# Kernel tuning notes

Measured on AMD Instinct MI355X. Metric: run time of the kernel, lower is better.

## Reference

```python
import jax, jax.numpy as jnp
import numpy as np

T, B, L, D, A = 64, 64, 100, 128, 18
H = 4 * D  # lstm_size = 4 * input_size


def lstm_cell(x, h, c, Wih, Whh, bih, bhh):
    # PyTorch LSTM gate order: i, f, g, o
    g = x @ Wih.T + bih + h @ Whh.T + bhh
    i, f, gg, o = jnp.split(g, 4, axis=-1)
    c = jax.nn.sigmoid(f) * c + jax.nn.sigmoid(i) * jnp.tanh(gg)
    h = jax.nn.sigmoid(o) * jnp.tanh(c)
    return h, c


def setup_inputs() -> dict:
    key = jax.random.key(0)
    ks = jax.random.split(key, 26)

    def gl(k, shape, fan_in):
        s = float(1.0 / np.sqrt(fan_in))
        return jax.random.uniform(k, shape, jnp.float32, -s, s)

    return dict(
        state=jax.random.normal(ks[0], (T, B, D), jnp.float32),
        demonstration=jax.random.normal(ks[1], (T, B, L, D), jnp.float32),
        demonstration_length=jax.random.randint(ks[2], (T, B), 1, L + 1),
        prev_action=jax.random.randint(ks[3], (T, B), 0, A),
        prev_reward=jax.random.normal(ks[4], (T, B), jnp.float32),
        h0=jnp.zeros((B, H), jnp.float32),
        c0=jnp.zeros((B, H), jnp.float32),
        enc_Wih=gl(ks[5], (4 * H, D), H), enc_Whh=gl(ks[6], (4 * H, H), H),
        enc_bih=gl(ks[7], (4 * H,), H), enc_bhh=gl(ks[8], (4 * H,), H),
        attn_W=gl(ks[9], (H, H), H), attn_b=gl(ks[10], (H,), H),
        comb_W=gl(ks[11], (H, D + H), D + H), comb_b=gl(ks[12], (H,), D + H),
        lstm_Wih=gl(ks[13], (4 * H, H), H), lstm_Whh=gl(ks[14], (4 * H, H), H),
        lstm_bih=gl(ks[15], (4 * H,), H), lstm_bhh=gl(ks[16], (4 * H,), H),
        mid_W=gl(ks[17], (H, H), H), mid_b=gl(ks[18], (H,), H),
        out_W=gl(ks[19], (A, H), H), out_b=gl(ks[20], (A,), H),
    )


def reference(state, demonstration, demonstration_length, prev_action, prev_reward,
              h0, c0, enc_Wih, enc_Whh, enc_bih, enc_bhh, attn_W, attn_b,
              comb_W, comb_b, lstm_Wih, lstm_Whh, lstm_bih, lstm_bhh,
              mid_W, mid_b, out_W, out_b):
    Lm = demonstration.shape[2]
    demo0 = demonstration[0]  # [B, L, D] (source uses demonstration[0] only)

    # --- demonstration encoder LSTM over L, zero initial state ---
    def enc_step(carry, x):
        h, c = carry
        h, c = lstm_cell(x, h, c, enc_Wih, enc_Whh, enc_bih, enc_bhh)
        return (h, c), h

    z = jnp.zeros((demo0.shape[0], H), demo0.dtype)
    _, enc = jax.lax.scan(enc_step, (z, z), jnp.swapaxes(demo0, 0, 1))
    enc = jnp.swapaxes(enc, 0, 1)  # [B, L, H]

    # invariant across t in the source loop; hoisted (same math)
    attn_proj = enc @ attn_W.T + attn_b  # [B, L, H]
    lengths = demonstration_length[0]  # [B]
    mask = jnp.arange(Lm)[None, :] < lengths[:, None]  # [B, L]
    scale = jnp.float32(1.0 / np.sqrt(Lm))

    # --- per-timestep fused attention + LSTM cell + heads ---
    def step(carry, obs_t):
        h, c = carry
        w = jnp.einsum('blh,bh->bl', attn_proj, h) * scale
        w = jnp.where(mask, w, -jnp.inf)
        w = jax.nn.softmax(w, axis=-1)
        applied = jnp.einsum('bl,blh->bh', w, enc)
        x = jax.nn.relu(jnp.concatenate([applied, obs_t], axis=-1) @ comb_W.T + comb_b)
        h, c = lstm_cell(x, h, c, lstm_Wih, lstm_Whh, lstm_bih, lstm_bhh)
        m = h @ mid_W.T + mid_b
        q_t = m @ out_W.T + out_b
        return (h, c), q_t

    (h, c), q = jax.lax.scan(step, (h0, c0), state)  # q: [T, B, A]
    return q, h, c
```

## Files before the change

kernel.cpp:

```cpp
#include <hip/hip_runtime.h>
#include <math.h>

#define Bsz 64
#define Tn 64
#define Ln 100
#define Dn 128
#define An 18
#define Hn 512
#define NGRP 16

__device__ __forceinline__ float sigf(float x){ return 1.0f/(1.0f+expf(-x)); }

__device__ __forceinline__ void scst(float* p, float v){
  __hip_atomic_store(p, v, __ATOMIC_RELAXED, __HIP_MEMORY_SCOPE_AGENT);
}
__device__ __forceinline__ void scsti(int* p, int v){
  __hip_atomic_store(p, v, __ATOMIC_RELAXED, __HIP_MEMORY_SCOPE_AGENT);
}
__device__ __forceinline__ int lcldi(const int* p){
  return __hip_atomic_load((int*)p, __ATOMIC_RELAXED, __HIP_MEMORY_SCOPE_AGENT);
}

__device__ __forceinline__ void gbar_arrive(int* grp_arr, int* grp_gen, int* root, int nb, int ph){
  const int gs = nb >> 4;
  const int g  = (int)blockIdx.x & 15;
  int a = __hip_atomic_fetch_add(grp_arr + g*64, 1, __ATOMIC_RELAXED, __HIP_MEMORY_SCOPE_AGENT) + 1;
  if (a == ph*gs){
    int r = __hip_atomic_fetch_add(root, 1, __ATOMIC_RELAXED, __HIP_MEMORY_SCOPE_AGENT) + 1;
    if (r == ph*NGRP){
      #pragma unroll
      for (int i = 0; i < NGRP; i++) scsti(grp_gen + i*64, ph);
    }
  }
}
__device__ __forceinline__ void gbar_wait(int* grp_gen, int ph){
  const int g = (int)blockIdx.x & 15;
  while (lcldi(grp_gen + g*64) < ph) __builtin_amdgcn_s_sleep(1);
}
__device__ __forceinline__ void gbarH(int* gA, int* gG, int* gR, int nb, int ph){
  __syncthreads();
  if (threadIdx.x == 0){
    asm volatile("s_waitcnt vmcnt(0) lgkmcnt(0)" ::: "memory");
    gbar_arrive(gA, gG, gR, nb, ph);
    gbar_wait(gG, ph);
  }
  __syncthreads();
}

__global__ __launch_bounds__(256) void demo_transpose_kernel(
    const float* __restrict__ demo, float* __restrict__ demoT)
{
  int idx = blockIdx.x*256 + threadIdx.x;
  if (idx < Ln*Bsz*Dn) {
    int d = idx & 127;
    int b = (idx >> 7) & 63;
    int l = idx >> 13;
    demoT[idx] = demo[((size_t)(b*Ln + l))*Dn + d];
  }
}

__global__ __launch_bounds__(256) void gemm_nt_kernel(
    const float* __restrict__ A, int lda,
    const float* __restrict__ B, int ldb,
    const float* __restrict__ bias,
    float* __restrict__ C, int ldc, int K)
{
  __shared__ float As[64][17];
  __shared__ float Bs[64][17];
  const int m0 = blockIdx.x * 64;
  const int n0 = blockIdx.y * 64;
  const int tx = threadIdx.x & 15;
  const int ty = threadIdx.x >> 4;
  float acc[4][4] = {};
  for (int k0 = 0; k0 < K; k0 += 16) {
    #pragma unroll
    for (int i = 0; i < 4; i++) {
      int e = threadIdx.x + i*256;
      int r = e >> 4, c = e & 15;
      As[r][c] = A[(size_t)(m0 + r)*lda + k0 + c];
      Bs[r][c] = B[(size_t)(n0 + r)*ldb + k0 + c];
    }
    __syncthreads();
    #pragma unroll
    for (int kk = 0; kk < 16; kk++) {
      float a0 = As[ty*4+0][kk], a1 = As[ty*4+1][kk], a2 = As[ty*4+2][kk], a3 = As[ty*4+3][kk];
      float b0 = Bs[tx*4+0][kk], b1 = Bs[tx*4+1][kk], b2 = Bs[tx*4+2][kk], b3 = Bs[tx*4+3][kk];
      acc[0][0] += a0*b0; acc[0][1] += a0*b1; acc[0][2] += a0*b2; acc[0][3] += a0*b3;
      acc[1][0] += a1*b0; acc[1][1] += a1*b1; acc[1][2] += a1*b2; acc[1][3] += a1*b3;
      acc[2][0] += a2*b0; acc[2][1] += a2*b1; acc[2][2] += a2*b2; acc[2][3] += a2*b3;
      acc[3][0] += a3*b0; acc[3][1] += a3*b1; acc[3][2] += a3*b2; acc[3][3] += a3*b3;
    }
    __syncthreads();
  }
  #pragma unroll
  for (int i = 0; i < 4; i++) {
    #pragma unroll
    for (int j = 0; j < 4; j++) {
      int nn = n0 + tx*4 + j;
      float v = acc[i][j] + (bias ? bias[nn] : 0.0f);
      C[(size_t)(m0 + ty*4 + i)*ldc + nn] = v;
    }
  }
}

__global__ __launch_bounds__(512) void head_fold_kernel(
    const float* __restrict__ mid_W, const float* __restrict__ mid_b,
    const float* __restrict__ out_W, const float* __restrict__ out_b,
    float* __restrict__ M2, float* __restrict__ bias2)
{
  const int a = blockIdx.x;
  const int k = threadIdx.x;
  const float* ow = out_W + (size_t)a*Hn;
  float s = 0.f;
  #pragma unroll 4
  for (int n = 0; n < Hn; n++) s += ow[n]*mid_W[(size_t)n*Hn + k];
  M2[(size_t)a*Hn + k] = s;
  if (k == 0){
    float b2 = out_b[a];
    for (int n = 0; n < Hn; n++) b2 += ow[n]*mid_b[n];
    bias2[a] = b2;
  }
}

__global__ __launch_bounds__(256) void qhead_kernel(
    const float* __restrict__ hhist, const float* __restrict__ M2,
    const float* __restrict__ bias2, float* __restrict__ q)
{
  const int t = blockIdx.x;
  for (int p = threadIdx.x; p < Bsz*An; p += 256){
    int b = p / An, a = p % An;
    const float4* hv = (const float4*)(hhist + ((size_t)t*Bsz + b)*Hn);
    const float4* mv = (const float4*)(M2 + (size_t)a*Hn);
    float s = bias2[a];
    #pragma unroll 8
    for (int k = 0; k < Hn/4; k++){
      float4 H = hv[k], M = mv[k];
      s += H.x*M.x + H.y*M.y + H.z*M.z + H.w*M.w;
    }
    q[((size_t)(t*Bsz + b))*An + a] = s;
  }
}

__global__ __launch_bounds__(512, 1) void enc_scan_kernel(
    const float* __restrict__ demoT,
    const float* __restrict__ Wih, const float* __restrict__ Whh,
    const float* __restrict__ bih, const float* __restrict__ bhh,
    const float* __restrict__ attn_W, const float* __restrict__ attn_b,
    const float* __restrict__ comb_W,
    float* __restrict__ hencR,
    float* __restrict__ attnp,
    float* __restrict__ CE,
    int* __restrict__ gA, int* __restrict__ gG, int* __restrict__ gR)
{
  const int bid  = blockIdx.x;
  const int tid  = threadIdx.x;
  const int lane = tid & 63;
  const int ks   = tid >> 6;
  const int n0   = bid*2;

  __shared__ float lds_whh[8][Hn];
  __shared__ float lds_wih[8][Dn];
  __shared__ float lds_atw[2][Hn];
  __shared__ float lds_cbw[2][Hn];
  __shared__ float red[8][12][Bsz];

  #pragma unroll
  for (int c = 0; c < 2; c++)
    #pragma unroll
    for (int g = 0; g < 4; g++){
      int r = c*4 + g;
      lds_whh[r][tid] = Whh[(size_t)(g*Hn + n0 + c)*Hn + tid];
      if (tid < Dn) lds_wih[r][tid] = Wih[(size_t)(g*Hn + n0 + c)*Dn + tid];
    }
  #pragma unroll
  for (int c = 0; c < 2; c++){
    lds_atw[c][tid] = attn_W[(size_t)(n0 + c)*Hn + tid];
    lds_cbw[c][tid] = comb_W[(size_t)(n0 + c)*(Hn + Dn) + tid];
  }
  float bsum[2][4];
  #pragma unroll
  for (int c = 0; c < 2; c++)
    #pragma unroll
    for (int g = 0; g < 4; g++){
      int r = g*Hn + n0 + c;
      bsum[c][g] = bih[r] + bhh[r];
    }
  const float ab[2] = { attn_b[n0], attn_b[n0+1] };
  float cr[2] = {0.f, 0.f};
  __syncthreads();

  for (int l = 0; l <= Ln; l++){
    if (l < Ln){
      float a[2][4] = {{0,0,0,0},{0,0,0,0}};
      if (l >= 1){
        const float4* hv = (const float4*)(hencR + ((size_t)(l-1)*Bsz + lane)*Hn) + ks*16;
        #pragma unroll 4
        for (int q = 0; q < 16; q++){
          float4 H = hv[q];
          #pragma unroll
          for (int c = 0; c < 2; c++)
            #pragma unroll
            for (int g = 0; g < 4; g++){
              float4 W = *(const float4*)&lds_whh[c*4+g][ks*64 + 4*q];
              a[c][g] += H.x*W.x + H.y*W.y + H.z*W.z + H.w*W.w;
            }
        }
      }
      {
        const float4* dv = (const float4*)(demoT + ((size_t)l*Bsz + lane)*Dn) + ks*4;
        #pragma unroll
        for (int q = 0; q < 4; q++){
          float4 V = dv[q];
          #pragma unroll
          for (int c = 0; c < 2; c++)
            #pragma unroll
            for (int g = 0; g < 4; g++){
              float4 W = *(const float4*)&lds_wih[c*4+g][ks*16 + 4*q];
              a[c][g] += V.x*W.x + V.y*W.y + V.z*W.z + V.w*W.w;
            }
        }
      }
      #pragma unroll
      for (int c = 0; c < 2; c++)
        #pragma unroll
        for (int g = 0; g < 4; g++) red[ks][c*4+g][lane] = a[c][g];
      __syncthreads();
      if (tid < Bsz){
        int b = tid;
        #pragma unroll
        for (int c = 0; c < 2; c++){
          float g0 = bsum[c][0], g1 = bsum[c][1], g2 = bsum[c][2], g3 = bsum[c][3];
          #pragma unroll
          for (int k = 0; k < 8; k++){
            g0 += red[k][c*4+0][b]; g1 += red[k][c*4+1][b];
            g2 += red[k][c*4+2][b]; g3 += red[k][c*4+3][b];
          }
          float ii = sigf(g0), ff = sigf(g1), gg = tanhf(g2), oo = sigf(g3);
          float cn = ff*cr[c] + ii*gg;
          float hn = oo*tanhf(cn);
          cr[c] = cn;
          scst(hencR + ((size_t)l*Bsz + b)*Hn + n0 + c, hn);
        }
      }
      if (tid == 0){
        asm volatile("s_waitcnt vmcnt(0)" ::: "memory");
        gbar_arrive(gA, gG, gR, (int)gridDim.x, l+1);
      }
    }
    if (l >= 1){
      float aa[2] = {0,0}, ac[2] = {0,0};
      const float4* hv = (const float4*)(hencR + ((size_t)(l-1)*Bsz + lane)*Hn) + ks*16;
      #pragma unroll 4
      for (int q = 0; q < 16; q++){
        float4 H = hv[q];
        #pragma unroll
        for (int c = 0; c < 2; c++){
          float4 Aw = *(const float4*)&lds_atw[c][ks*64 + 4*q];
          aa[c] += H.x*Aw.x + H.y*Aw.y + H.z*Aw.z + H.w*Aw.w;
          float4 Cw = *(const float4*)&lds_cbw[c][ks*64 + 4*q];
          ac[c] += H.x*Cw.x + H.y*Cw.y + H.z*Cw.z + H.w*Cw.w;
        }
      }
      #pragma unroll
      for (int c = 0; c < 2; c++){
        red[ks][8+c][lane]  = aa[c];
        red[ks][10+c][lane] = ac[c];
      }
      __syncthreads();
      if (tid < Bsz){
        int b = tid;
        #pragma unroll
        for (int c = 0; c < 2; c++){
          float av = ab[c], cv = 0.f;
          #pragma unroll
          for (int k = 0; k < 8; k++){ av += red[k][8+c][b]; cv += red[k][10+c][b]; }
          scst(attnp + ((size_t)(b*Ln + (l-1)))*Hn + n0 + c, av);
          scst(CE    + ((size_t)(b*Ln + (l-1)))*Hn + n0 + c, cv);
        }
      }
    }
    if (l < Ln){
      if (tid == 0) gbar_wait(gG, l+1);
      __syncthreads();
    }
  }
}

__global__ __launch_bounds__(512, 1) void dec_scan_kernel(
    const float* __restrict__ h0, const float* __restrict__ c0,
    const float* __restrict__ attnp,
    const float* __restrict__ CE,
    const float* __restrict__ preobs,
    const int*   __restrict__ dlen,
    const float* __restrict__ lstm_Wih, const float* __restrict__ lstm_Whh,
    const float* __restrict__ lstm_bih, const float* __restrict__ lstm_bhh,
    const float* __restrict__ comb_b,
    float* __restrict__ xrow,
    float* __restrict__ hhist,
    float* __restrict__ outp,
    int* __restrict__ gA, int* __restrict__ gG, int* __restrict__ gR)
{
  const int bid  = blockIdx.x;
  const int tid  = threadIdx.x;
  const int lane = tid & 63;
  const int ks   = tid >> 6;
  const int n0   = bid*2;

  __shared__ float lds_wi[8][Hn];
  __shared__ float lds_wh[8][Hn];
  __shared__ float hs[Hn];
  __shared__ float wls[128];
  __shared__ float mx_s, sum_s;
  __shared__ float red[8][8][Bsz];

  #pragma unroll
  for (int c = 0; c < 2; c++)
    #pragma unroll
    for (int g = 0; g < 4; g++){
      int r = c*4 + g;
      lds_wi[r][tid] = lstm_Wih[(size_t)(g*Hn + n0 + c)*Hn + tid];
      lds_wh[r][tid] = lstm_Whh[(size_t)(g*Hn + n0 + c)*Hn + tid];
    }
  float bs[2][4];
  #pragma unroll
  for (int c = 0; c < 2; c++)
    #pragma unroll
    for (int g = 0; g < 4; g++){
      int r = g*Hn + n0 + c;
      bs[c][g] = lstm_bih[r] + lstm_bhh[r];
    }
  float cr[2] = {0.f, 0.f};
  int ph = 0;
  __syncthreads();

  for (int t = 0; t < Tn; t++){
    const float* hprev_all = (t == 0) ? h0 : (hhist + (size_t)(t-1)*Bsz*Hn);

    if (bid < Bsz){
      const int b = bid;
      hs[tid] = hprev_all[(size_t)b*Hn + tid];
      if (tid >= 100 && tid < 128) wls[tid] = -1e30f;
      __syncthreads();
      const int len = dlen[b];
      if (tid < 400){
        int l = tid >> 2, kh = tid & 3;
        const float4* ap = (const float4*)(attnp + ((size_t)(b*Ln + l))*Hn) + kh*32;
        const float4* hv = (const float4*)hs + kh*32;
        float s = 0.f;
        #pragma unroll 8
        for (int k = 0; k < 32; k++){
          float4 A = ap[k], H = hv[k];
          s += A.x*H.x + A.y*H.y + A.z*H.z + A.w*H.w;
        }
        s += __shfl_xor(s, 1);
        s += __shfl_xor(s, 2);
        if (kh == 0) wls[l] = (l < len) ? s*0.1f : -1e30f;
      }
      __syncthreads();
      if (tid < 64){
        float v = fmaxf(wls[tid], wls[tid+64]);
        for (int off = 1; off < 64; off <<= 1) v = fmaxf(v, __shfl_xor(v, off));
        if (tid == 0) mx_s = v;
      }
      __syncthreads();
      float mx = mx_s;
      if (tid < 64){
        float e0 = (wls[tid]    > -1e29f) ? expf(wls[tid]    - mx) : 0.f;
        float e1 = (wls[tid+64] > -1e29f) ? expf(wls[tid+64] - mx) : 0.f;
        wls[tid] = e0; wls[tid+64] = e1;
        float v = e0 + e1;
        for (int off = 1; off < 64; off <<= 1) v += __shfl_xor(v, off);
        if (tid == 0) sum_s = v;
      }
      __syncthreads();
      float inv = 1.0f / sum_s;
      {
        int n = tid;
        const float* cb = CE + (size_t)b*Ln*Hn + n;
        float acc = 0.f;
        #pragma unroll 4
        for (int l2 = 0; l2 < Ln; ++l2) acc += cb[(size_t)l2*Hn]*wls[l2];
        float v = acc*inv + preobs[((size_t)(t*Bsz + b))*Hn + n] + comb_b[n];
        scst(xrow + ((size_t)t*Bsz + b)*Hn + n, fmaxf(v, 0.f));
      }
    }
    float hpa[2][4] = {{0,0,0,0},{0,0,0,0}};
    {
      const float4* hv = (const float4*)(hprev_all + (size_t)lane*Hn) + ks*16;
      #pragma unroll 4
      for (int q = 0; q < 16; q++){
        float4 H = hv[q];
        #pragma unroll
        for (int c = 0; c < 2; c++)
          #pragma unroll
          for (int g = 0; g < 4; g++){
            float4 W = *(const float4*)&lds_wh[c*4+g][ks*64 + 4*q];
            hpa[c][g] += H.x*W.x + H.y*W.y + H.z*W.z + H.w*W.w;
          }
      }
    }
    gbarH(gA, gG, gR, (int)gridDim.x, ++ph);

    {
      const float4* xv = (const float4*)(xrow + ((size_t)t*Bsz + lane)*Hn) + ks*16;
      #pragma unroll 4
      for (int q = 0; q < 16; q++){
        float4 X = xv[q];
        #pragma unroll
        for (int c = 0; c < 2; c++)
          #pragma unroll
          for (int g = 0; g < 4; g++){
            float4 W = *(const float4*)&lds_wi[c*4+g][ks*64 + 4*q];
            hpa[c][g] += X.x*W.x + X.y*W.y + X.z*W.z + X.w*W.w;
          }
      }
      #pragma unroll
      for (int c = 0; c < 2; c++)
        #pragma unroll
        for (int g = 0; g < 4; g++) red[ks][c*4+g][lane] = hpa[c][g];
      __syncthreads();
      if (tid < Bsz){
        int b = tid;
        #pragma unroll
        for (int c = 0; c < 2; c++){
          int n = n0 + c;
          if (t == 0) cr[c] = c0[(size_t)b*Hn + n];
          float g0 = bs[c][0], g1 = bs[c][1], g2 = bs[c][2], g3 = bs[c][3];
          #pragma unroll
          for (int k = 0; k < 8; k++){
            g0 += red[k][c*4+0][b]; g1 += red[k][c*4+1][b];
            g2 += red[k][c*4+2][b]; g3 += red[k][c*4+3][b];
          }
          float ii = sigf(g0), ff = sigf(g1), gg = tanhf(g2), oo = sigf(g3);
          float cn = ff*cr[c] + ii*gg;
          float hn = oo*tanhf(cn);
          cr[c] = cn;
          scst(hhist + ((size_t)t*Bsz + b)*Hn + n, hn);
          if (t == Tn - 1){
            outp[Tn*Bsz*An + (size_t)b*Hn + n]           = hn;
            outp[Tn*Bsz*An + Bsz*Hn + (size_t)b*Hn + n]  = cn;
          }
        }
      }
      if (t < Tn - 1){
        if (tid == 0){
          asm volatile("s_waitcnt vmcnt(0)" ::: "memory");
          gbar_arrive(gA, gG, gR, (int)gridDim.x, ph+1);
          gbar_wait(gG, ph+1);
        }
        ph++;
        __syncthreads();
      }
    }
  }
}

extern "C" void kernel_launch(void* const* d_in, const int* in_sizes, int n_in,
                              void* d_out, int out_size, void* d_ws, size_t ws_size,
                              hipStream_t stream) {
  (void)in_sizes; (void)n_in; (void)out_size; (void)ws_size;
  const float* state    = (const float*)d_in[0];
  const float* demo     = (const float*)d_in[1];
  const int*   dlen     = (const int*)  d_in[2];
  const float* h0       = (const float*)d_in[5];
  const float* c0       = (const float*)d_in[6];
  const float* enc_Wih  = (const float*)d_in[7];
  const float* enc_Whh  = (const float*)d_in[8];
  const float* enc_bih  = (const float*)d_in[9];
  const float* enc_bhh  = (const float*)d_in[10];
  const float* attn_W   = (const float*)d_in[11];
  const float* attn_b   = (const float*)d_in[12];
  const float* comb_W   = (const float*)d_in[13];
  const float* comb_b   = (const float*)d_in[14];
  const float* lstm_Wih = (const float*)d_in[15];
  const float* lstm_Whh = (const float*)d_in[16];
  const float* lstm_bih = (const float*)d_in[17];
  const float* lstm_bhh = (const float*)d_in[18];
  const float* mid_W    = (const float*)d_in[19];
  const float* mid_b    = (const float*)d_in[20];
  const float* out_W    = (const float*)d_in[21];
  const float* out_b    = (const float*)d_in[22];
  float* ws   = (float*)d_ws;
  float* qout = (float*)d_out;

  float* attnp  = ws + 0;
  float* CE     = ws + 3276800;
  float* preobs = ws + 6553600;
  float* region = ws + 8650752;
  float* demoT  = region;
  float* hencR  = region + 819200;
  float* xrow   = region;
  float* hhist  = region + 2097152;
  int*   barB   = (int*)(ws + 12845056);
  int* encA = barB;          int* encG = barB + 1024; int* encR = barB + 2048;
  int* decA = barB + 2112;   int* decG = barB + 3136; int* decR = barB + 4160;
  float* M2    = ws + 12850176;
  float* bias2 = ws + 12859392;

  hipMemsetAsync((void*)barB, 0, 4224*4, stream);

  demo_transpose_kernel<<<3200, 256, 0, stream>>>(demo, demoT);

  head_fold_kernel<<<An, 512, 0, stream>>>(mid_W, mid_b, out_W, out_b, M2, bias2);

  gemm_nt_kernel<<<dim3(Tn*Bsz/64, Hn/64), 256, 0, stream>>>(
      state, Dn, comb_W + Hn, Hn + Dn, nullptr, preobs, Hn, Dn);

  enc_scan_kernel<<<256, 512, 0, stream>>>(
      demoT, enc_Wih, enc_Whh, enc_bih, enc_bhh, attn_W, attn_b, comb_W,
      hencR, attnp, CE, encA, encG, encR);

  dec_scan_kernel<<<256, 512, 0, stream>>>(
      h0, c0, attnp, CE, preobs, dlen, lstm_Wih, lstm_Whh, lstm_bih, lstm_bhh,
      comb_b, xrow, hhist, qout, decA, decG, decR);

  qhead_kernel<<<Tn, 256, 0, stream>>>(hhist, M2, bias2, qout);
}
```

Measured before the change: 3.418 ms.

## Split decoder attention across 128 blocks with partial softmax merge; fuse encoder projections

In the decoder, the attention and context computation for each batch row is split over two blocks, each handling 50 positions. Each block writes a partial max, denominator and weighted context, and these are merged flash-style when the LSTM input is built after the grid barrier. This halves the serial attention work per block that sits before the barrier, at the cost of extra global traffic and redundant merging in every block. In the encoder, the attention and combine projections of the previous step are folded into the same h-vector pass as the recurrent matmul. That removes one h reload and one __syncthreads per step.

```diff
diff --git a/kernel.cpp b/kernel.cpp
--- a/kernel.cpp
+++ b/kernel.cpp
@@ -190,93 +190,79 @@
   __syncthreads();
 
   for (int l = 0; l <= Ln; l++){
-    if (l < Ln){
-      float a[2][4] = {{0,0,0,0},{0,0,0,0}};
-      if (l >= 1){
-        const float4* hv = (const float4*)(hencR + ((size_t)(l-1)*Bsz + lane)*Hn) + ks*16;
-        #pragma unroll 4
-        for (int q = 0; q < 16; q++){
-          float4 H = hv[q];
-          #pragma unroll
-          for (int c = 0; c < 2; c++)
-            #pragma unroll
-            for (int g = 0; g < 4; g++){
-              float4 W = *(const float4*)&lds_whh[c*4+g][ks*64 + 4*q];
-              a[c][g] += H.x*W.x + H.y*W.y + H.z*W.z + H.w*W.w;
-            }
-        }
-      }
-      {
-        const float4* dv = (const float4*)(demoT + ((size_t)l*Bsz + lane)*Dn) + ks*4;
-        #pragma unroll
-        for (int q = 0; q < 4; q++){
-          float4 V = dv[q];
-          #pragma unroll
-          for (int c = 0; c < 2; c++)
-            #pragma unroll
-            for (int g = 0; g < 4; g++){
-              float4 W = *(const float4*)&lds_wih[c*4+g][ks*16 + 4*q];
-              a[c][g] += V.x*W.x + V.y*W.y + V.z*W.z + V.w*W.w;
-            }
-        }
-      }
-      #pragma unroll
-      for (int c = 0; c < 2; c++)
-        #pragma unroll
-        for (int g = 0; g < 4; g++) red[ks][c*4+g][lane] = a[c][g];
-      __syncthreads();
-      if (tid < Bsz){
-        int b = tid;
-        #pragma unroll
-        for (int c = 0; c < 2; c++){
-          float g0 = bsum[c][0], g1 = bsum[c][1], g2 = bsum[c][2], g3 = bsum[c][3];
-          #pragma unroll
-          for (int k = 0; k < 8; k++){
-            g0 += red[k][c*4+0][b]; g1 += red[k][c*4+1][b];
-            g2 += red[k][c*4+2][b]; g3 += red[k][c*4+3][b];
-          }
-          float ii = sigf(g0), ff = sigf(g1), gg = tanhf(g2), oo = sigf(g3);
-          float cn = ff*cr[c] + ii*gg;
-          float hn = oo*tanhf(cn);
-          cr[c] = cn;
-          scst(hencR + ((size_t)l*Bsz + b)*Hn + n0 + c, hn);
-        }
-      }
-      if (tid == 0){
-        asm volatile("s_waitcnt vmcnt(0)" ::: "memory");
-        gbar_arrive(gA, gG, gR, (int)gridDim.x, l+1);
-      }
-    }
+    float a[2][4] = {{0,0,0,0},{0,0,0,0}};
+    float aa[2] = {0,0}, ac[2] = {0,0};
     if (l >= 1){
-      float aa[2] = {0,0}, ac[2] = {0,0};
       const float4* hv = (const float4*)(hencR + ((size_t)(l-1)*Bsz + lane)*Hn) + ks*16;
       #pragma unroll 4
       for (int q = 0; q < 16; q++){
         float4 H = hv[q];
         #pragma unroll
         for (int c = 0; c < 2; c++){
+          #pragma unroll
+          for (int g = 0; g < 4; g++){
+            float4 W = *(const float4*)&lds_whh[c*4+g][ks*64 + 4*q];
+            a[c][g] += H.x*W.x + H.y*W.y + H.z*W.z + H.w*W.w;
+          }
           float4 Aw = *(const float4*)&lds_atw[c][ks*64 + 4*q];
           aa[c] += H.x*Aw.x + H.y*Aw.y + H.z*Aw.z + H.w*Aw.w;
           float4 Cw = *(const float4*)&lds_cbw[c][ks*64 + 4*q];
           ac[c] += H.x*Cw.x + H.y*Cw.y + H.z*Cw.z + H.w*Cw.w;
         }
       }
+    }
+    if (l < Ln){
+      const float4* dv = (const float4*)(demoT + ((size_t)l*Bsz + lane)*Dn) + ks*4;
+      #pragma unroll
+      for (int q = 0; q < 4; q++){
+        float4 V = dv[q];
+        #pragma unroll
+        for (int c = 0; c < 2; c++)
+          #pragma unroll
+          for (int g = 0; g < 4; g++){
+            float4 W = *(const float4*)&lds_wih[c*4+g][ks*16 + 4*q];
+            a[c][g] += V.x*W.x + V.y*W.y + V.z*W.z + V.w*W.w;
+          }
+      }
+    }
+    #pragma unroll
+    for (int c = 0; c < 2; c++){
+      #pragma unroll
+      for (int g = 0; g < 4; g++) red[ks][c*4+g][lane] = a[c][g];
+      red[ks][8+c][lane]  = aa[c];
+      red[ks][10+c][lane] = ac[c];
+    }
+    __syncthreads();
+    if (tid < Bsz && l < Ln){
+      int b = tid;
       #pragma unroll
       for (int c = 0; c < 2; c++){
-        red[ks][8+c][lane]  = aa[c];
-        red[ks][10+c][lane] = ac[c];
-      }
-      __syncthreads();
-      if (tid < Bsz){
-        int b = tid;
-        #pragma unroll
-        for (int c = 0; c < 2; c++){
-          float av = ab[c], cv = 0.f;
-          #pragma unroll
-          for (int k = 0; k < 8; k++){ av += red[k][8+c][b]; cv += red[k][10+c][b]; }
-          scst(attnp + ((size_t)(b*Ln + (l-1)))*Hn + n0 + c, av);
-          scst(CE    + ((size_t)(b*Ln + (l-1)))*Hn + n0 + c, cv);
+        float g0 = bsum[c][0], g1 = bsum[c][1], g2 = bsum[c][2], g3 = bsum[c][3];
+        #pragma unroll
+        for (int k = 0; k < 8; k++){
+          g0 += red[k][c*4+0][b]; g1 += red[k][c*4+1][b];
+          g2 += red[k][c*4+2][b]; g3 += red[k][c*4+3][b];
         }
+        float ii = sigf(g0), ff = sigf(g1), gg = tanhf(g2), oo = sigf(g3);
+        float cn = ff*cr[c] + ii*gg;
+        float hn = oo*tanhf(cn);
+        cr[c] = cn;
+        scst(hencR + ((size_t)l*Bsz + b)*Hn + n0 + c, hn);
+      }
+    }
+    if (l < Ln && tid == 0){
+      asm volatile("s_waitcnt vmcnt(0)" ::: "memory");
+      gbar_arrive(gA, gG, gR, (int)gridDim.x, l+1);
+    }
+    if (tid < Bsz && l >= 1){
+      int b = tid;
+      #pragma unroll
+      for (int c = 0; c < 2; c++){
+        float av = ab[c], cv = 0.f;
+        #pragma unroll
+        for (int k = 0; k < 8; k++){ av += red[k][8+c][b]; cv += red[k][10+c][b]; }
+        scst(attnp + ((size_t)(b*Ln + (l-1)))*Hn + n0 + c, av);
+        scst(CE    + ((size_t)(b*Ln + (l-1)))*Hn + n0 + c, cv);
       }
     }
     if (l < Ln){
@@ -295,7 +281,9 @@
     const float* __restrict__ lstm_Wih, const float* __restrict__ lstm_Whh,
     const float* __restrict__ lstm_bih, const float* __restrict__ lstm_bhh,
     const float* __restrict__ comb_b,
-    float* __restrict__ xrow,
+    float* __restrict__ app,
+    float* __restrict__ dmax,
+    float* __restrict__ dden,
     float* __restrict__ hhist,
     float* __restrict__ outp,
     int* __restrict__ gA, int* __restrict__ gG, int* __restrict__ gR)
@@ -309,8 +297,9 @@
   __shared__ float lds_wi[8][Hn];
   __shared__ float lds_wh[8][Hn];
   __shared__ float hs[Hn];
-  __shared__ float wls[128];
-  __shared__ float mx_s, sum_s;
+  __shared__ float cbs[Hn];
+  __shared__ float sls[64];
+  __shared__ float wls[64];
   __shared__ float red[8][8][Bsz];
 
   #pragma unroll
@@ -321,6 +310,7 @@
       lds_wi[r][tid] = lstm_Wih[(size_t)(g*Hn + n0 + c)*Hn + tid];
       lds_wh[r][tid] = lstm_Whh[(size_t)(g*Hn + n0 + c)*Hn + tid];
     }
+  cbs[tid] = comb_b[tid];
   float bs[2][4];
   #pragma unroll
   for (int c = 0; c < 2; c++)
@@ -333,57 +323,14 @@
   int ph = 0;
   __syncthreads();
 
+  const int batn = bid & 63;
+  const int qq   = bid >> 6;
+
   for (int t = 0; t < Tn; t++){
     const float* hprev_all = (t == 0) ? h0 : (hhist + (size_t)(t-1)*Bsz*Hn);
 
-    if (bid < Bsz){
-      const int b = bid;
-      hs[tid] = hprev_all[(size_t)b*Hn + tid];
-      if (tid >= 100 && tid < 128) wls[tid] = -1e30f;
-      __syncthreads();
-      const int len = dlen[b];
-      if (tid < 400){
-        int l = tid >> 2, kh = tid & 3;
-        const float4* ap = (const float4*)(attnp + ((size_t)(b*Ln + l))*Hn) + kh*32;
-        const float4* hv = (const float4*)hs + kh*32;
-        float s = 0.f;
-        #pragma unroll 8
-        for (int k = 0; k < 32; k++){
-          float4 A = ap[k], H = hv[k];
-          s += A.x*H.x + A.y*H.y + A.z*H.z + A.w*H.w;
-        }
-        s += __shfl_xor(s, 1);
-        s += __shfl_xor(s, 2);
-        if (kh == 0) wls[l] = (l < len) ? s*0.1f : -1e30f;
-      }
-      __syncthreads();
-      if (tid < 64){
-        float v = fmaxf(wls[tid], wls[tid+64]);
-        for (int off = 1; off < 64; off <<= 1) v = fmaxf(v, __shfl_xor(v, off));
-        if (tid == 0) mx_s = v;
-      }
-      __syncthreads();
-      float mx = mx_s;
-      if (tid < 64){
-        float e0 = (wls[tid]    > -1e29f) ? expf(wls[tid]    - mx) : 0.f;
-        float e1 = (wls[tid+64] > -1e29f) ? expf(wls[tid+64] - mx) : 0.f;
-        wls[tid] = e0; wls[tid+64] = e1;
-        float v = e0 + e1;
-        for (int off = 1; off < 64; off <<= 1) v += __shfl_xor(v, off);
-        if (tid == 0) sum_s = v;
-      }
-      __syncthreads();
-      float inv = 1.0f / sum_s;
-      {
-        int n = tid;
-        const float* cb = CE + (size_t)b*Ln*Hn + n;
-        float acc = 0.f;
-        #pragma unroll 4
-        for (int l2 = 0; l2 < Ln; ++l2) acc += cb[(size_t)l2*Hn]*wls[l2];
-        float v = acc*inv + preobs[((size_t)(t*Bsz + b))*Hn + n] + comb_b[n];
-        scst(xrow + ((size_t)t*Bsz + b)*Hn + n, fmaxf(v, 0.f));
-      }
-    }
+    if (bid < 128) hs[tid] = hprev_all[(size_t)batn*Hn + tid];
+
     float hpa[2][4] = {{0,0,0,0},{0,0,0,0}};
     {
       const float4* hv = (const float4*)(hprev_all + (size_t)lane*Hn) + ks*16;
@@ -399,13 +346,77 @@
           }
       }
     }
+
+    if (bid < 128){
+      const int b = batn;
+      const int l0 = qq*50;
+      __syncthreads();
+      const int len = dlen[b];
+      const int li = tid >> 3, sub = tid & 7;
+      float s = -1e30f;
+      if (li < 50){
+        const float4* ap = (const float4*)(attnp + ((size_t)(b*Ln + l0 + li))*Hn) + sub*16;
+        const float4* hv2 = (const float4*)hs + sub*16;
+        float acc = 0.f;
+        #pragma unroll
+        for (int k = 0; k < 16; k++){
+          float4 A = ap[k], H = hv2[k];
+          acc += A.x*H.x + A.y*H.y + A.z*H.z + A.w*H.w;
+        }
+        acc += __shfl_xor(acc, 1);
+        acc += __shfl_xor(acc, 2);
+        acc += __shfl_xor(acc, 4);
+        s = acc;
+      }
+      if (sub == 0) sls[li] = (li < 50 && (l0 + li) < len) ? s*0.1f : -1e30f;
+      __syncthreads();
+      if (tid < 64){
+        float v = sls[tid];
+        float m = v;
+        #pragma unroll
+        for (int off = 1; off < 64; off <<= 1) m = fmaxf(m, __shfl_xor(m, off));
+        float w = expf(v - m);
+        wls[tid] = w;
+        float dsum = w;
+        #pragma unroll
+        for (int off = 1; off < 64; off <<= 1) dsum += __shfl_xor(dsum, off);
+        if (tid == 0){
+          scst(dmax + ((size_t)t*2 + qq)*Bsz + b, m);
+          scst(dden + ((size_t)t*2 + qq)*Bsz + b, dsum);
+        }
+      }
+      __syncthreads();
+      {
+        const int n = tid;
+        const float* ceb = CE + ((size_t)(b*Ln + l0))*Hn + n;
+        float apv = 0.f;
+        #pragma unroll 5
+        for (int l2 = 0; l2 < 50; l2++) apv += wls[l2]*ceb[(size_t)l2*Hn];
+        scst(app + (((size_t)t*2 + qq)*Bsz + b)*Hn + n, apv);
+      }
+    }
     gbarH(gA, gG, gR, (int)gridDim.x, ++ph);
 
     {
-      const float4* xv = (const float4*)(xrow + ((size_t)t*Bsz + lane)*Hn) + ks*16;
+      const size_t i0 = ((size_t)t*2 + 0)*Bsz + lane;
+      const size_t i1 = ((size_t)t*2 + 1)*Bsz + lane;
+      float m0 = dmax[i0], m1 = dmax[i1], d0v = dden[i0], d1v = dden[i1];
+      float M  = fmaxf(m0, m1);
+      float e0 = expf(m0 - M), e1 = expf(m1 - M);
+      float D  = e0*d0v + e1*d1v;
+      float s0 = e0/D, s1 = e1/D;
+      const float4* a0v = (const float4*)(app + i0*Hn) + ks*16;
+      const float4* a1v = (const float4*)(app + i1*Hn) + ks*16;
+      const float4* pv  = (const float4*)(preobs + ((size_t)t*Bsz + lane)*Hn) + ks*16;
       #pragma unroll 4
       for (int q = 0; q < 16; q++){
-        float4 X = xv[q];
+        float4 A0 = a0v[q], A1 = a1v[q], P = pv[q];
+        float4 CB = *(const float4*)&cbs[ks*64 + 4*q];
+        float4 X;
+        X.x = fmaxf(s0*A0.x + s1*A1.x + P.x + CB.x, 0.f);
+        X.y = fmaxf(s0*A0.y + s1*A1.y + P.y + CB.y, 0.f);
+        X.z = fmaxf(s0*A0.z + s1*A1.z + P.z + CB.z, 0.f);
+        X.w = fmaxf(s0*A0.w + s1*A1.w + P.w + CB.w, 0.f);
         #pragma unroll
         for (int c = 0; c < 2; c++)
           #pragma unroll
@@ -489,13 +500,15 @@
   float* region = ws + 8650752;
   float* demoT  = region;
   float* hencR  = region + 819200;
-  float* xrow   = region;
-  float* hhist  = region + 2097152;
-  int*   barB   = (int*)(ws + 12845056);
+  float* hhist  = region;
+  float* app    = region + 2097152;
+  float* dmax   = region + 6291456;
+  float* dden   = region + 6299648;
+  int*   barB   = (int*)(ws + 14958592);
   int* encA = barB;          int* encG = barB + 1024; int* encR = barB + 2048;
   int* decA = barB + 2112;   int* decG = barB + 3136; int* decR = barB + 4160;
-  float* M2    = ws + 12850176;
-  float* bias2 = ws + 12859392;
+  float* M2    = ws + 14962816;
+  float* bias2 = ws + 14972032;
 
   hipMemsetAsync((void*)barB, 0, 4224*4, stream);
 
@@ -512,7 +525,7 @@
 
   dec_scan_kernel<<<256, 512, 0, stream>>>(
       h0, c0, attnp, CE, preobs, dlen, lstm_Wih, lstm_Whh, lstm_bih, lstm_bhh,
-      comb_b, xrow, hhist, qout, decA, decG, decR);
+      comb_b, app, dmax, dden, hhist, qout, decA, decG, decR);
 
   qhead_kernel<<<Tn, 256, 0, stream>>>(hhist, M2, bias2, qout);
 }
```

After: 3.178 ms. -7.0%, faster.

## Merge encoder projection pass into recurrence step and trim attention loop to length

Applied to the files above, without the earlier changes.

In the encoder scan, the attention and combine projections of h_{l-1} are now computed in the same pass over h as the recurrent matvec. This removes one extra __syncthreads and one reload of h per step, and both results share one reduction. Both scans now use a gbarH helper for the grid barrier. The decoder's weighted sum over the encoder outputs stops at the demonstration length rounded up to a multiple of 8 instead of all 100 positions, with a deeper unroll. The workspace layout is changed so the buffers no longer alias, which adds memory footprint.

```diff
diff --git a/kernel.cpp b/kernel.cpp
--- a/kernel.cpp
+++ b/kernel.cpp
@@ -190,43 +190,52 @@
   __syncthreads();
 
   for (int l = 0; l <= Ln; l++){
+    float a[2][4] = {{0,0,0,0},{0,0,0,0}};
+    float aa[2] = {0,0}, ac[2] = {0,0};
+    if (l >= 1){
+      const float4* hv = (const float4*)(hencR + ((size_t)(l-1)*Bsz + lane)*Hn) + ks*16;
+      #pragma unroll 4
+      for (int q = 0; q < 16; q++){
+        float4 H = hv[q];
+        #pragma unroll
+        for (int c = 0; c < 2; c++){
+          #pragma unroll
+          for (int g = 0; g < 4; g++){
+            float4 W = *(const float4*)&lds_whh[c*4+g][ks*64 + 4*q];
+            a[c][g] += H.x*W.x + H.y*W.y + H.z*W.z + H.w*W.w;
+          }
+          float4 Aw = *(const float4*)&lds_atw[c][ks*64 + 4*q];
+          aa[c] += H.x*Aw.x + H.y*Aw.y + H.z*Aw.z + H.w*Aw.w;
+          float4 Cw = *(const float4*)&lds_cbw[c][ks*64 + 4*q];
+          ac[c] += H.x*Cw.x + H.y*Cw.y + H.z*Cw.z + H.w*Cw.w;
+        }
+      }
+    }
     if (l < Ln){
-      float a[2][4] = {{0,0,0,0},{0,0,0,0}};
-      if (l >= 1){
-        const float4* hv = (const float4*)(hencR + ((size_t)(l-1)*Bsz + lane)*Hn) + ks*16;
-        #pragma unroll 4
-        for (int q = 0; q < 16; q++){
-          float4 H = hv[q];
-          #pragma unroll
-          for (int c = 0; c < 2; c++)
-            #pragma unroll
-            for (int g = 0; g < 4; g++){
-              float4 W = *(const float4*)&lds_whh[c*4+g][ks*64 + 4*q];
-              a[c][g] += H.x*W.x + H.y*W.y + H.z*W.z + H.w*W.w;
-            }
-        }
-      }
-      {
-        const float4* dv = (const float4*)(demoT + ((size_t)l*Bsz + lane)*Dn) + ks*4;
-        #pragma unroll
-        for (int q = 0; q < 4; q++){
-          float4 V = dv[q];
-          #pragma unroll
-          for (int c = 0; c < 2; c++)
-            #pragma unroll
-            for (int g = 0; g < 4; g++){
-              float4 W = *(const float4*)&lds_wih[c*4+g][ks*16 + 4*q];
-              a[c][g] += V.x*W.x + V.y*W.y + V.z*W.z + V.w*W.w;
-            }
-        }
-      }
+      const float4* dv = (const float4*)(demoT + ((size_t)l*Bsz + lane)*Dn) + ks*4;
       #pragma unroll
-      for (int c = 0; c < 2; c++)
-        #pragma unroll
-        for (int g = 0; g < 4; g++) red[ks][c*4+g][lane] = a[c][g];
-      __syncthreads();
-      if (tid < Bsz){
-        int b = tid;
+      for (int q = 0; q < 4; q++){
+        float4 V = dv[q];
+        #pragma unroll
+        for (int c = 0; c < 2; c++)
+          #pragma unroll
+          for (int g = 0; g < 4; g++){
+            float4 W = *(const float4*)&lds_wih[c*4+g][ks*16 + 4*q];
+            a[c][g] += V.x*W.x + V.y*W.y + V.z*W.z + V.w*W.w;
+          }
+      }
+    }
+    #pragma unroll
+    for (int c = 0; c < 2; c++){
+      #pragma unroll
+      for (int g = 0; g < 4; g++) red[ks][c*4+g][lane] = a[c][g];
+      red[ks][8+c][lane]  = aa[c];
+      red[ks][10+c][lane] = ac[c];
+    }
+    __syncthreads();
+    if (tid < Bsz){
+      int b = tid;
+      if (l < Ln){
         #pragma unroll
         for (int c = 0; c < 2; c++){
           float g0 = bsum[c][0], g1 = bsum[c][1], g2 = bsum[c][2], g3 = bsum[c][3];
@@ -242,33 +251,7 @@
           scst(hencR + ((size_t)l*Bsz + b)*Hn + n0 + c, hn);
         }
       }
-      if (tid == 0){
-        asm volatile("s_waitcnt vmcnt(0)" ::: "memory");
-        gbar_arrive(gA, gG, gR, (int)gridDim.x, l+1);
-      }
-    }
-    if (l >= 1){
-      float aa[2] = {0,0}, ac[2] = {0,0};
-      const float4* hv = (const float4*)(hencR + ((size_t)(l-1)*Bsz + lane)*Hn) + ks*16;
-      #pragma unroll 4
-      for (int q = 0; q < 16; q++){
-        float4 H = hv[q];
-        #pragma unroll
-        for (int c = 0; c < 2; c++){
-          float4 Aw = *(const float4*)&lds_atw[c][ks*64 + 4*q];
-          aa[c] += H.x*Aw.x + H.y*Aw.y + H.z*Aw.z + H.w*Aw.w;
-          float4 Cw = *(const float4*)&lds_cbw[c][ks*64 + 4*q];
-          ac[c] += H.x*Cw.x + H.y*Cw.y + H.z*Cw.z + H.w*Cw.w;
-        }
-      }
-      #pragma unroll
-      for (int c = 0; c < 2; c++){
-        red[ks][8+c][lane]  = aa[c];
-        red[ks][10+c][lane] = ac[c];
-      }
-      __syncthreads();
-      if (tid < Bsz){
-        int b = tid;
+      if (l >= 1){
         #pragma unroll
         for (int c = 0; c < 2; c++){
           float av = ab[c], cv = 0.f;
@@ -279,10 +262,7 @@
         }
       }
     }
-    if (l < Ln){
-      if (tid == 0) gbar_wait(gG, l+1);
-      __syncthreads();
-    }
+    if (l < Ln) gbarH(gA, gG, gR, (int)gridDim.x, l+1);
   }
 }
 
@@ -330,6 +310,8 @@
       bs[c][g] = lstm_bih[r] + lstm_bhh[r];
     }
   float cr[2] = {0.f, 0.f};
+  int len = 0, lenr = 0;
+  if (bid < Bsz){ len = dlen[bid]; lenr = (len + 7) & ~7; }
   int ph = 0;
   __syncthreads();
 
@@ -341,7 +323,6 @@
       hs[tid] = hprev_all[(size_t)b*Hn + tid];
       if (tid >= 100 && tid < 128) wls[tid] = -1e30f;
       __syncthreads();
-      const int len = dlen[b];
       if (tid < 400){
         int l = tid >> 2, kh = tid & 3;
         const float4* ap = (const float4*)(attnp + ((size_t)(b*Ln + l))*Hn) + kh*32;
@@ -378,8 +359,8 @@
         int n = tid;
         const float* cb = CE + (size_t)b*Ln*Hn + n;
         float acc = 0.f;
-        #pragma unroll 4
-        for (int l2 = 0; l2 < Ln; ++l2) acc += cb[(size_t)l2*Hn]*wls[l2];
+        #pragma unroll 8
+        for (int l2 = 0; l2 < lenr; ++l2) acc += cb[(size_t)l2*Hn]*wls[l2];
         float v = acc*inv + preobs[((size_t)(t*Bsz + b))*Hn + n] + comb_b[n];
         scst(xrow + ((size_t)t*Bsz + b)*Hn + n, fmaxf(v, 0.f));
       }
@@ -442,16 +423,8 @@
           }
         }
       }
-      if (t < Tn - 1){
-        if (tid == 0){
-          asm volatile("s_waitcnt vmcnt(0)" ::: "memory");
-          gbar_arrive(gA, gG, gR, (int)gridDim.x, ph+1);
-          gbar_wait(gG, ph+1);
-        }
-        ph++;
-        __syncthreads();
-      }
-    }
+    }
+    if (t < Tn - 1) gbarH(gA, gG, gR, (int)gridDim.x, ++ph);
   }
 }
 
@@ -485,17 +458,16 @@
 
   float* attnp  = ws + 0;
   float* CE     = ws + 3276800;
-  float* preobs = ws + 6553600;
-  float* region = ws + 8650752;
-  float* demoT  = region;
-  float* hencR  = region + 819200;
-  float* xrow   = region;
-  float* hhist  = region + 2097152;
-  int*   barB   = (int*)(ws + 12845056);
+  float* preobs = ws + 6555648;
+  float* demoT  = ws + 8652800;
+  float* hencR  = ws + 9472000;
+  float* xrow   = ws + 12748800;
+  float* hhist  = ws + 14845952;
+  int*   barB   = (int*)(ws + 16943104);
   int* encA = barB;          int* encG = barB + 1024; int* encR = barB + 2048;
   int* decA = barB + 2112;   int* decG = barB + 3136; int* decR = barB + 4160;
-  float* M2    = ws + 12850176;
-  float* bias2 = ws + 12859392;
+  float* M2    = ws + 16947328;
+  float* bias2 = ws + 16956544;
 
   hipMemsetAsync((void*)barB, 0, 4224*4, stream);
 
```

Result: faster. 2.835 ms (-17.1%).
